# Performance work log

Hardware: AMD Instinct MI355X
Metric: run time of the kernel (lower is better)

Reference implementation:

```python
import jax, jax.numpy as jnp
import numpy as np

# Hyperparameters from module __init__
U_TH = 1.0      # firing threshold
BETA = 0.5      # membrane decay
BATCH_SIZE = 128
DELTA = 0.05    # ZO smoothing radius


def setup_inputs() -> dict:
    key = jax.random.key(0)
    k1, k2 = jax.random.split(key)
    T, B, F = 32, BATCH_SIZE, 8192
    inputs = jax.random.normal(k1, (T * B, F), dtype=jnp.float32)
    # 'sample once' Gaussian ZO tangents, same shape as inputs
    random_tangents = jax.random.normal(k2, (T * B, F), dtype=jnp.float32)
    return {"inputs": inputs, "random_tangents": random_tangents}


def reference(inputs, random_tangents):
    """Leaky integrate-and-fire over time with LocalZO (single-sample)
    surrogate gradient. inputs: [T*B, F] with T = leading//BATCH_SIZE."""
    orig_shape = inputs.shape
    T = inputs.shape[0] // BATCH_SIZE
    x = inputs.reshape(T, BATCH_SIZE, *inputs.shape[1:])
    z = random_tangents.reshape(T, BATCH_SIZE, *inputs.shape[1:])

    def step(u, xt_zt):
        xt, zt = xt_zt
        u = BETA * u + xt                      # membrane update
        v = u - U_TH                           # distance to threshold
        # LocalZO single-sample surrogate: |z|/(2*delta) * 1(|v| < delta*|z|)
        surr = jax.lax.stop_gradient(
            (jnp.abs(zt) / (2.0 * DELTA))
            * (jnp.abs(v) < DELTA * jnp.abs(zt)).astype(xt.dtype)
        )
        h = (v > 0).astype(xt.dtype)           # hard spike
        # straight-through: forward = h, d spike / d v = surr
        spike = jax.lax.stop_gradient(h - surr * v) + surr * v
        u = u - spike * U_TH                   # soft reset (subtract threshold)
        return u, spike

    u0 = jnp.zeros_like(x[0])
    _, spikes = jax.lax.scan(step, u0, (x, z))
    return spikes.reshape(orig_shape)
```

## Files before the change

### kernel.cpp

```cpp
#include <hip/hip_runtime.h>


constexpr int BATCH = 128;
constexpr int FDIM  = 8192;
constexpr int STEP  = BATCH * FDIM;
constexpr int VEC   = 4;

__global__ __launch_bounds__(256) void lif_zo_kernel(
    const float* __restrict__ x,
    const float* __restrict__ z,
    float* __restrict__ out,
    int T)
{
#pragma clang fp contract(off)
    const int tid = blockIdx.x * blockDim.x + threadIdx.x;
    long idx = (long)tid * VEC;

    float u[VEC];
#pragma unroll
    for (int c = 0; c < VEC; ++c) u[c] = 0.0f;

    for (int t = 0; t < T; ++t, idx += STEP) {
        const float4 xt = *reinterpret_cast<const float4*>(x + idx);
        const float4 zt = *reinterpret_cast<const float4*>(z + idx);
        const float xs[VEC] = {xt.x, xt.y, xt.z, xt.w};
        const float zs[VEC] = {zt.x, zt.y, zt.z, zt.w};
        float ss[VEC];
#pragma unroll
        for (int c = 0; c < VEC; ++c) {
            float uu = 0.5f * u[c];
            uu = uu + xs[c];
            float v = uu - 1.0f;
            float az   = fabsf(zs[c]);
            float thr  = 0.05f * az;
            float ind  = (fabsf(v) < thr) ? 1.0f : 0.0f;
            float surr = (az / 0.1f) * ind;
            float h = (v > 0.0f) ? 1.0f : 0.0f;
            float a     = surr * v;
            float spike = (h - a) + a;
            u[c] = uu - spike * 1.0f;
            ss[c] = spike;
        }
        const float4 s4 = make_float4(ss[0], ss[1], ss[2], ss[3]);
        *reinterpret_cast<float4*>(out + idx) = s4;
    }
}

extern "C" void kernel_launch(void* const* d_in, const int* in_sizes, int n_in,
                              void* d_out, int out_size, void* d_ws, size_t ws_size,
                              hipStream_t stream)
{
    const float* x = (const float*)d_in[0];
    const float* z = (const float*)d_in[1];
    float* out = (float*)d_out;

    const int total = in_sizes[0];
    const int T = total / STEP;

    const int nthreads = STEP / VEC;
    const int block = 256;
    const int grid = nthreads / block;

    lif_zo_kernel<<<grid, block, 0, stream>>>(x, z, out, T);
}
```

Measured before the change: 306.5 us.

## Halve per-thread width, prefetch next timestep, use nontemporal stores

Switches each thread from four to two features, so the grid doubles in size and there are more waves in flight. Loads for timestep t+1 are issued before timestep t is computed, a software prefetch that hides memory latency across the serial time loop. Output is written with nontemporal stores to avoid polluting the cache. The trade-offs are narrower 8-byte accesses instead of 16-byte ones and one redundant reload on the final iteration.

```diff
diff --git a/kernel.cpp b/kernel.cpp
--- a/kernel.cpp
+++ b/kernel.cpp
@@ -4,7 +4,24 @@
 constexpr int BATCH = 128;
 constexpr int FDIM  = 8192;
 constexpr int STEP  = BATCH * FDIM;
-constexpr int VEC   = 4;
+constexpr int VEC   = 2;
+
+typedef float f32x2 __attribute__((ext_vector_type(2)));
+
+__device__ __forceinline__ float lif_step(float& u, float xs, float zs)
+{
+    float uu = 0.5f * u;
+    uu = uu + xs;
+    float v = uu - 1.0f;
+    float az   = fabsf(zs);
+    float ind  = (fabsf(v) < 0.05f * az) ? 1.0f : 0.0f;
+    float surr = (az / 0.1f) * ind;
+    float h    = (v > 0.0f) ? 1.0f : 0.0f;
+    float a     = surr * v;
+    float spike = (h - a) + a;
+    u = uu - spike * 1.0f;
+    return spike;
+}
 
 __global__ __launch_bounds__(256) void lif_zo_kernel(
     const float* __restrict__ x,
@@ -16,33 +33,25 @@
     const int tid = blockIdx.x * blockDim.x + threadIdx.x;
     long idx = (long)tid * VEC;
 
-    float u[VEC];
-#pragma unroll
-    for (int c = 0; c < VEC; ++c) u[c] = 0.0f;
+    float u0 = 0.0f, u1 = 0.0f;
 
-    for (int t = 0; t < T; ++t, idx += STEP) {
-        const float4 xt = *reinterpret_cast<const float4*>(x + idx);
-        const float4 zt = *reinterpret_cast<const float4*>(z + idx);
-        const float xs[VEC] = {xt.x, xt.y, xt.z, xt.w};
-        const float zs[VEC] = {zt.x, zt.y, zt.z, zt.w};
-        float ss[VEC];
-#pragma unroll
-        for (int c = 0; c < VEC; ++c) {
-            float uu = 0.5f * u[c];
-            uu = uu + xs[c];
-            float v = uu - 1.0f;
-            float az   = fabsf(zs[c]);
-            float thr  = 0.05f * az;
-            float ind  = (fabsf(v) < thr) ? 1.0f : 0.0f;
-            float surr = (az / 0.1f) * ind;
-            float h = (v > 0.0f) ? 1.0f : 0.0f;
-            float a     = surr * v;
-            float spike = (h - a) + a;
-            u[c] = uu - spike * 1.0f;
-            ss[c] = spike;
-        }
-        const float4 s4 = make_float4(ss[0], ss[1], ss[2], ss[3]);
-        *reinterpret_cast<float4*>(out + idx) = s4;
+    f32x2 xt = *reinterpret_cast<const f32x2*>(x + idx);
+    f32x2 zt = *reinterpret_cast<const f32x2*>(z + idx);
+
+    for (int t = 0; t < T; ++t) {
+        const long nidx = idx + ((t + 1 < T) ? (long)STEP : 0);
+        f32x2 xn = *reinterpret_cast<const f32x2*>(x + nidx);
+        f32x2 zn = *reinterpret_cast<const f32x2*>(z + nidx);
+
+        f32x2 s;
+        s.x = lif_step(u0, xt.x, zt.x);
+        s.y = lif_step(u1, xt.y, zt.y);
+
+        __builtin_nontemporal_store(s, reinterpret_cast<f32x2*>(out + idx));
+
+        idx = idx + STEP;
+        xt = xn;
+        zt = zn;
     }
 }
 
```

New measurement: 322.4 us. 5.2% more time.
